# Kernel optimization log

Hardware: AMD Instinct MI355X
Metric: run time of the kernel (lower is better)

## Reference

```python
import jax, jax.numpy as jnp
import numpy as np

HEADS = 12
IDX = 0


def setup_inputs() -> dict:
    key = jax.random.key(0)
    ks = jax.random.split(key, 6)
    B, H, W, C = 16, 64, 64, 384
    x = jax.random.normal(ks[0], (B, H * W, C), dtype=jnp.float32)
    qkv_w = jax.random.normal(ks[1], (3 * C, C), dtype=jnp.float32) * 0.02
    proj_w = jax.random.normal(ks[2], (C, C), dtype=jnp.float32) * 0.02
    proj_b = jax.random.normal(ks[3], (C,), dtype=jnp.float32) * 0.02
    lepe_w = jax.random.normal(ks[4], (C, 1, 3, 3), dtype=jnp.float32) * 0.02  # depthwise, torch OIHW with I=1
    lepe_b = jax.random.normal(ks[5], (C,), dtype=jnp.float32) * 0.02
    return {"x": x, "qkv_w": qkv_w, "proj_w": proj_w, "proj_b": proj_b,
            "lepe_w": lepe_w, "lepe_b": lepe_b, "H": H, "W": W}


def _lepe_forward(x, qkv_w, proj_w, proj_b, lepe_w, lepe_b, H, W):
    B, N, C = x.shape
    hd = C // HEADS
    scale = hd ** (-0.5)
    x_img = x.reshape(B, H, W, C)

    if IDX == 0:
        # vertical strips: attend over H within each column
        x_split = jnp.transpose(x_img, (0, 2, 1, 3)).reshape(B * W, H, C)
    else:
        x_split = x_img.reshape(B * H, W, C)
    S, L, _ = x_split.shape

    qkv = (x_split @ qkv_w.T).reshape(S, L, 3, HEADS, hd)
    qkv = jnp.transpose(qkv, (2, 0, 3, 1, 4))  # (3, S, heads, L, hd)
    q, k, v = qkv[0], qkv[1], qkv[2]

    attn = jnp.einsum('shld,shmd->shlm', q, k) * scale
    attn = jax.nn.softmax(attn, axis=-1)
    out = jnp.einsum('shlm,shmd->shld', attn, v)           # (S, heads, L, hd)
    out = jnp.transpose(out, (0, 2, 1, 3)).reshape(S, L, C)
    # faithful to torch: view(B, out_H, out_W, C).view(B, H*W, C) -- no permute back for idx==0
    out_flat = out.reshape(B, H * W, C)

    # depthwise 3x3 conv LePE on the original (H, W) layout
    lepe = jax.lax.conv_general_dilated(
        jnp.transpose(x_img, (0, 3, 1, 2)), lepe_w,
        window_strides=(1, 1), padding='SAME',
        feature_group_count=C,
        dimension_numbers=('NCHW', 'OIHW', 'NCHW'))
    lepe = lepe + lepe_b[None, :, None, None]
    lepe = jnp.transpose(lepe, (0, 2, 3, 1)).reshape(B, H * W, C)

    return (out_flat + lepe) @ proj_w.T + proj_b


def reference(x, qkv_w, proj_w, proj_b, lepe_w, lepe_b, H, W):
    return _lepe_forward(x, qkv_w, proj_w, proj_b, lepe_w, lepe_b, H, W)
```

## Files before the change

### kernel.cpp

```cpp
#include <hip/hip_runtime.h>


typedef _Float16 f16;
typedef _Float16 f16x2 __attribute__((ext_vector_type(2)));
typedef _Float16 f16x8 __attribute__((ext_vector_type(8)));
typedef float    f32x4 __attribute__((ext_vector_type(4)));

__device__ __forceinline__ f32x4 mfma_16x16x32(f16x8 a, f16x8 b, f32x4 c) {
  return __builtin_amdgcn_mfma_f32_16x16x32_f16(a, b, c, 0, 0, 0);
}

__device__ __forceinline__ void gl_lds16(const f16* g, f16* l) {
  __builtin_amdgcn_global_load_lds((const __attribute__((address_space(1))) void*)g,
                                   (__attribute__((address_space(3))) void*)l, 16, 0, 0);
}

__global__ __launch_bounds__(256) void k_cvt(const float* __restrict__ src,
                                             f16* __restrict__ dst, int n8) {
  int i = blockIdx.x * 256 + threadIdx.x;
  if (i >= n8) return;
  const f32x4* s4 = (const f32x4*)src;
  f32x4 a = s4[2 * i], b = s4[2 * i + 1];
  f16x8 o;
#pragma unroll
  for (int j = 0; j < 4; ++j) { o[j] = (f16)a[j]; o[4 + j] = (f16)b[j]; }
  *(f16x8*)&dst[(long)i * 8] = o;
}

__global__ __launch_bounds__(256) void k_prep(const float* __restrict__ x,
                                              const float* __restrict__ lw,
                                              const float* __restrict__ lb,
                                              f16* __restrict__ x16,
                                              f16* __restrict__ lepe16) {
  __shared__ float ws[9 * 384];
  __shared__ float bs[384];
  for (int i = threadIdx.x; i < 3456; i += 256) {
    int c = i / 9, tap = i - c * 9;
    ws[tap * 384 + (c & 7) * 48 + (c >> 3)] = lw[i];
  }
  for (int i = threadIdx.x; i < 384; i += 256)
    bs[(i & 7) * 48 + (i >> 3)] = lb[i];
  __syncthreads();

  int chunk = blockIdx.x * 256 + threadIdx.x;
  int token = chunk / 48;
  int c0 = (chunk - token * 48) * 8;
  int cg = c0 >> 3;
  int b = token >> 12, n = token & 4095, h = n >> 6, w = n & 63;
  const float* xb = x + (long)(b << 12) * 384;

  float a8[8];
#pragma unroll
  for (int cc = 0; cc < 8; ++cc) a8[cc] = bs[cc * 48 + cg];
  f16x8 cv;
#pragma unroll
  for (int ky = 0; ky < 3; ++ky) {
    int hh = h + ky - 1;
    if (hh < 0 || hh > 63) continue;
#pragma unroll
    for (int kx = 0; kx < 3; ++kx) {
      int ww = w + kx - 1;
      if (ww < 0 || ww > 63) continue;
      const float* p = xb + (long)((hh << 6) + ww) * 384 + c0;
      float4 u = *(const float4*)p;
      float4 v = *(const float4*)(p + 4);
      float xs[8] = {u.x, u.y, u.z, u.w, v.x, v.y, v.z, v.w};
      if (ky == 1 && kx == 1) {
#pragma unroll
        for (int cc = 0; cc < 8; ++cc) cv[cc] = (f16)xs[cc];
      }
      int tap = ky * 3 + kx;
#pragma unroll
      for (int cc = 0; cc < 8; ++cc)
        a8[cc] += xs[cc] * ws[tap * 384 + cc * 48 + cg];
    }
  }
  f16x8 o;
#pragma unroll
  for (int cc = 0; cc < 8; ++cc) o[cc] = (f16)a8[cc];
  *(f16x8*)&x16[(long)token * 384 + c0] = cv;
  *(f16x8*)&lepe16[(long)token * 384 + c0] = o;
}

__global__ __launch_bounds__(512) void k_qkv(const f16* __restrict__ A,
                                             const f16* __restrict__ Bt,
                                             f16* __restrict__ C) {
  __shared__ alignas(16) f16 smem[49152];
  f16* ebuf = smem;
  const int tid = threadIdx.x;
  const int lane = tid & 63;
  const int wave = tid >> 6;
  const int wr = wave >> 1, wc = wave & 1;
  const int ln = lane & 15, quad = lane >> 4;
  const int bid = blockIdx.x;
  const int xcd = bid & 7;
  const int s = bid >> 3;
  const int mq = s / 9;
  const int mt = xcd * 32 + mq;
  const int nt = s - mq * 9;
  const long m0 = (long)mt * 256;
  const int n0 = nt * 128;

  auto stage = [&](int buf, int k0) {
    f16* Asb = smem + buf * 16384;
    f16* Bsb = smem + 32768 + buf * 8192;
#pragma unroll
    for (int r = 0; r < 4; ++r) {
      int flat = r * 512 + tid;
      int row = flat >> 3, c8 = flat & 7;
      int sc8 = (c8 ^ (row & 7)) * 8;
      gl_lds16(&A[(m0 + row) * 384 + k0 + sc8], &Asb[flat * 8]);
    }
#pragma unroll
    for (int r = 0; r < 2; ++r) {
      int flat = r * 512 + tid;
      int row = flat >> 3, c8 = flat & 7;
      int sc8 = (c8 ^ (row & 7)) * 8;
      gl_lds16(&Bt[(long)(n0 + row) * 384 + k0 + sc8], &Bsb[flat * 8]);
    }
  };

  f32x4 acc[4][4] = {};
  stage(0, 0);
  __syncthreads();
  int cur = 0;
  for (int t = 0; t < 6; ++t) {
    if (t < 5) stage(cur ^ 1, (t + 1) * 64);
    const f16* Ac = smem + cur * 16384;
    const f16* Bc = smem + 32768 + cur * 8192;
#pragma unroll
    for (int ks = 0; ks < 2; ++ks) {
      f16x8 a[4], b[4];
#pragma unroll
      for (int i = 0; i < 4; ++i)
        a[i] = *(const f16x8*)&Ac[(wr * 64 + i * 16 + ln) * 64 +
                                  ((ks * 4 + quad) ^ (ln & 7)) * 8];
#pragma unroll
      for (int j = 0; j < 4; ++j)
        b[j] = *(const f16x8*)&Bc[(wc * 64 + j * 16 + ln) * 64 +
                                  ((ks * 4 + quad) ^ (ln & 7)) * 8];
#pragma unroll
      for (int i = 0; i < 4; ++i)
#pragma unroll
        for (int j = 0; j < 4; ++j)
          acc[i][j] = mfma_16x16x32(a[i], b[j], acc[i][j]);
    }
    __syncthreads();
    cur ^= 1;
  }

  for (int p = 0; p < 2; ++p) {
    if ((wr >> 1) == p) {
      const int lr0 = (wr & 1) * 64;
#pragma unroll
      for (int i = 0; i < 4; ++i)
#pragma unroll
        for (int j = 0; j < 4; ++j)
#pragma unroll
          for (int r = 0; r < 4; ++r)
            ebuf[(lr0 + i * 16 + quad * 4 + r) * 136 + wc * 64 + j * 16 + ln] =
                (f16)acc[i][j][r];
    }
    __syncthreads();
#pragma unroll
    for (int it = 0; it < 4; ++it) {
      int flat = it * 512 + tid;
      int row = flat >> 4;
      int c8 = flat & 15;
      int t = (int)m0 + p * 128 + row;
      int nn = t & 4095;
      long prow = (long)(t & ~4095) + ((nn & 63) << 6) + (nn >> 6);
      *(f16x8*)&C[prow * 1152 + n0 + c8 * 8] =
          *(const f16x8*)&ebuf[row * 136 + c8 * 8];
    }
    __syncthreads();
  }
}

__global__ __launch_bounds__(256, 2) void k_attnproj(const f16* __restrict__ qkv,
                                                     const f16* __restrict__ lepe16,
                                                     const f16* __restrict__ pw,
                                                     const float* __restrict__ bias,
                                                     float* __restrict__ outf) {
  __shared__ alignas(16) f16 shp[4][7424];
  __shared__ alignas(16) f16 aschunk[2][64 * 40];
  const int lane = threadIdx.x & 63;
  const int wave = threadIdx.x >> 6;
  const int ln = lane & 15, quad = lane >> 4, q8 = quad * 8;
  const int b = blockIdx.x >> 6, w = blockIdx.x & 63;
  const long sbase = (long)b * 4096 + (long)w * 64;

  f16* qs = shp[wave];
  f16* ks = shp[wave] + 2560;
  f16* vt = shp[wave] + 5120;
  f16* ps = shp[wave];
  const float qscale = 0.17677669529663687f;

  f16x2 ph0[16], ph1[16], ph2[16];

  for (int hi = 0; hi < 3; ++hi) {
    const int hh = wave * 3 + hi;
#pragma unroll
    for (int r = 0; r < 4; ++r) {
      int flat = r * 64 + lane;
      int l = flat >> 2, dg = (flat & 3) * 8;
      long ta = (sbase + l) * 1152 + hh * 32 + dg;
      f16x8 qv = *(const f16x8*)&qkv[ta];
      f16x8 kv = *(const f16x8*)&qkv[ta + 384];
      f16x8 vv = *(const f16x8*)&qkv[ta + 768];
#pragma unroll
      for (int ii = 0; ii < 8; ++ii) qv[ii] = (f16)((float)qv[ii] * qscale);
      *(f16x8*)&qs[l * 40 + dg] = qv;
      *(f16x8*)&ks[l * 40 + dg] = kv;
#pragma unroll
      for (int ii = 0; ii < 8; ++ii) vt[(dg + ii) * 72 + l] = vv[ii];
    }
    f16x8 aq[4], bk[4];
#pragma unroll
    for (int i = 0; i < 4; ++i) aq[i] = *(const f16x8*)&qs[(i * 16 + ln) * 40 + q8];
#pragma unroll
    for (int j = 0; j < 4; ++j) bk[j] = *(const f16x8*)&ks[(j * 16 + ln) * 40 + q8];
    f32x4 sc[4][4] = {};
#pragma unroll
    for (int i = 0; i < 4; ++i)
#pragma unroll
      for (int j = 0; j < 4; ++j) sc[i][j] = mfma_16x16x32(aq[i], bk[j], sc[i][j]);

    float rs[4][4];
#pragma unroll
    for (int i = 0; i < 4; ++i)
#pragma unroll
      for (int r = 0; r < 4; ++r) {
        float m = -1e30f;
#pragma unroll
        for (int j = 0; j < 4; ++j) m = fmaxf(m, sc[i][j][r]);
#pragma unroll
        for (int off = 1; off < 16; off <<= 1) m = fmaxf(m, __shfl_xor(m, off, 64));
        float sum = 0.f;
#pragma unroll
        for (int j = 0; j < 4; ++j) {
          float p = __expf(sc[i][j][r] - m);
          sc[i][j][r] = p;
          sum += p;
        }
#pragma unroll
        for (int off = 1; off < 16; off <<= 1) sum += __shfl_xor(sum, off, 64);
        rs[i][r] = 1.0f / sum;
      }

#pragma unroll
    for (int i = 0; i < 4; ++i)
#pragma unroll
      for (int j = 0; j < 4; ++j)
#pragma unroll
        for (int r = 0; r < 4; ++r)
          ps[(i * 16 + quad * 4 + r) * 72 + j * 16 + ln] = (f16)sc[i][j][r];

    f32x4 oc[4][2] = {};
#pragma unroll
    for (int k2 = 0; k2 < 2; ++k2) {
      f16x8 ap[4], bv[2];
#pragma unroll
      for (int i = 0; i < 4; ++i)
        ap[i] = *(const f16x8*)&ps[(i * 16 + ln) * 72 + k2 * 32 + q8];
#pragma unroll
      for (int j = 0; j < 2; ++j)
        bv[j] = *(const f16x8*)&vt[(j * 16 + ln) * 72 + k2 * 32 + q8];
#pragma unroll
      for (int i = 0; i < 4; ++i)
#pragma unroll
        for (int j = 0; j < 2; ++j) oc[i][j] = mfma_16x16x32(ap[i], bv[j], oc[i][j]);
    }

#pragma unroll
    for (int i = 0; i < 4; ++i)
#pragma unroll
      for (int r = 0; r < 4; ++r) {
        f16x2 pk;
        pk[0] = (f16)(oc[i][0][r] * rs[i][r]);
        pk[1] = (f16)(oc[i][1][r] * rs[i][r]);
        if (hi == 0) ph0[i * 4 + r] = pk;
        else if (hi == 1) ph1[i * 4 + r] = pk;
        else ph2[i * 4 + r] = pk;
      }
  }

#define WRITECHUNK(BI, PH)                                        \
  {                                                               \
    _Pragma("unroll") for (int i = 0; i < 4; ++i)                 \
        _Pragma("unroll") for (int r = 0; r < 4; ++r) {           \
      int row = i * 16 + quad * 4 + r;                            \
      aschunk[BI][row * 40 + ln] = PH[i * 4 + r][0];              \
      aschunk[BI][row * 40 + 16 + ln] = PH[i * 4 + r][1];         \
    }                                                             \
  }

  if (wave == 0) WRITECHUNK(0, ph0);
  __syncthreads();

  f32x4 pacc[4][6] = {};
  const int ncol0 = wave * 96;
#pragma unroll
  for (int c = 0; c < 12; ++c) {
    if (c + 1 < 12 && (c + 1) / 3 == wave) {
      const int h = (c + 1) % 3;
      if (h == 0) WRITECHUNK((c + 1) & 1, ph0)
      else if (h == 1) WRITECHUNK((c + 1) & 1, ph1)
      else WRITECHUNK((c + 1) & 1, ph2)
    }
    const f16* ac = aschunk[c & 1];
    f16x8 afr[4], bfr[6];
#pragma unroll
    for (int i = 0; i < 4; ++i) {
      f16x8 av = *(const f16x8*)&ac[(i * 16 + ln) * 40 + q8];
      f16x8 lv = *(const f16x8*)&lepe16[(sbase + i * 16 + ln) * 384 + c * 32 + q8];
      afr[i] = av + lv;
    }
#pragma unroll
    for (int j = 0; j < 6; ++j)
      bfr[j] = *(const f16x8*)&pw[(long)(ncol0 + j * 16 + ln) * 384 + c * 32 + q8];
#pragma unroll
    for (int i = 0; i < 4; ++i)
#pragma unroll
      for (int j = 0; j < 6; ++j)
        pacc[i][j] = mfma_16x16x32(afr[i], bfr[j], pacc[i][j]);
    __syncthreads();
  }
#undef WRITECHUNK

  float* ebuf = (float*)&shp[0][0];
#pragma unroll
  for (int p = 0; p < 2; ++p) {
    __syncthreads();
#pragma unroll
    for (int ii = 0; ii < 2; ++ii)
#pragma unroll
      for (int j = 0; j < 6; ++j)
#pragma unroll
        for (int r = 0; r < 4; ++r)
          ebuf[(ii * 16 + quad * 4 + r) * 388 + ncol0 + j * 16 + ln] =
              pacc[p * 2 + ii][j][r];
    __syncthreads();
#pragma unroll
    for (int it = 0; it < 12; ++it) {
      int flat = it * 256 + threadIdx.x;
      int row = flat / 96;
      int c4 = flat - row * 96;
      long gr = sbase + p * 32 + row;
      int col = c4 * 4;
      float4 b4 = *(const float4*)&bias[col];
      float4 o = *(const float4*)&ebuf[row * 388 + col];
      o.x += b4.x; o.y += b4.y; o.z += b4.z; o.w += b4.w;
      *(float4*)&outf[gr * 384 + col] = o;
    }
  }
}

extern "C" void kernel_launch(void* const* d_in, const int* in_sizes, int n_in,
                              void* d_out, int out_size, void* d_ws, size_t ws_size,
                              hipStream_t stream) {
  const float* x = (const float*)d_in[0];
  const float* qkv_w = (const float*)d_in[1];
  const float* proj_w = (const float*)d_in[2];
  const float* proj_b = (const float*)d_in[3];
  const float* lepe_w = (const float*)d_in[4];
  const float* lepe_b = (const float*)d_in[5];
  float* out = (float*)d_out;

  char* ws = (char*)d_ws;
  f16* w16 = (f16*)(ws + 0);
  f16* pw16 = (f16*)(ws + 884736);
  f16* x16 = (f16*)(ws + 1179648);
  f16* lepe16 = (f16*)(ws + 51511296);
  f16* qkv16 = (f16*)(ws + 101842944);

  k_cvt<<<216, 256, 0, stream>>>(qkv_w, w16, 55296);
  k_cvt<<<72, 256, 0, stream>>>(proj_w, pw16, 18432);
  k_prep<<<12288, 256, 0, stream>>>(x, lepe_w, lepe_b, x16, lepe16);
  k_qkv<<<2304, 512, 0, stream>>>(x16, w16, qkv16);
  k_attnproj<<<1024, 256, 0, stream>>>(qkv16, lepe16, pw16, proj_b, out);
}
```

Measured before the change: 461.1 us.

## Register-prefetch qkv and projection operands, swizzle V transpose, raise MFMA priority

The per-head q/k/v global loads are now double-buffered in registers, so the next head's data is fetched while the current head computes. The projection loop does the same for its lepe and weight fragments, prefetching the next K-chunk before the current MFMAs. The transposed V store in LDS gets an XOR swizzle on the sequence index to cut bank conflicts. The MFMA blocks are wrapped in s_setprio. All of this raises register pressure, which may lower occupancy or cause spills.

```diff
diff --git a/kernel.cpp b/kernel.cpp
--- a/kernel.cpp
+++ b/kernel.cpp
@@ -196,24 +196,48 @@
   f16* ps = shp[wave];
   const float qscale = 0.17677669529663687f;
 
+  const int lrow = lane >> 2;
+  const int ldg = (lane & 3) * 8;
+  const int lswz = lane & 3;
+
   f16x2 ph0[16], ph1[16], ph2[16];
 
+  f16x8 rq[2][4], rk[2][4], rv[2][4];
+#pragma unroll
+  for (int r = 0; r < 4; ++r) {
+    int l = r * 16 + lrow;
+    long ta = (sbase + l) * 1152 + (wave * 3) * 32 + ldg;
+    rq[0][r] = *(const f16x8*)&qkv[ta];
+    rk[0][r] = *(const f16x8*)&qkv[ta + 384];
+    rv[0][r] = *(const f16x8*)&qkv[ta + 768];
+  }
+
+#pragma unroll
   for (int hi = 0; hi < 3; ++hi) {
     const int hh = wave * 3 + hi;
+    const int cb = hi & 1;
 #pragma unroll
     for (int r = 0; r < 4; ++r) {
-      int flat = r * 64 + lane;
-      int l = flat >> 2, dg = (flat & 3) * 8;
-      long ta = (sbase + l) * 1152 + hh * 32 + dg;
-      f16x8 qv = *(const f16x8*)&qkv[ta];
-      f16x8 kv = *(const f16x8*)&qkv[ta + 384];
-      f16x8 vv = *(const f16x8*)&qkv[ta + 768];
+      int l = r * 16 + lrow;
+      f16x8 qv = rq[cb][r];
 #pragma unroll
       for (int ii = 0; ii < 8; ++ii) qv[ii] = (f16)((float)qv[ii] * qscale);
-      *(f16x8*)&qs[l * 40 + dg] = qv;
-      *(f16x8*)&ks[l * 40 + dg] = kv;
-#pragma unroll
-      for (int ii = 0; ii < 8; ++ii) vt[(dg + ii) * 72 + l] = vv[ii];
+      *(f16x8*)&qs[l * 40 + ldg] = qv;
+      *(f16x8*)&ks[l * 40 + ldg] = rk[cb][r];
+      int g = l >> 3, o = l & 7;
+#pragma unroll
+      for (int ii = 0; ii < 8; ++ii)
+        vt[(ldg + ii) * 72 + (((g ^ lswz) << 3) | o)] = rv[cb][r][ii];
+    }
+    if (hi < 2) {
+#pragma unroll
+      for (int r = 0; r < 4; ++r) {
+        int l = r * 16 + lrow;
+        long ta = (sbase + l) * 1152 + (hh + 1) * 32 + ldg;
+        rq[cb ^ 1][r] = *(const f16x8*)&qkv[ta];
+        rk[cb ^ 1][r] = *(const f16x8*)&qkv[ta + 384];
+        rv[cb ^ 1][r] = *(const f16x8*)&qkv[ta + 768];
+      }
     }
     f16x8 aq[4], bk[4];
 #pragma unroll
@@ -221,10 +245,12 @@
 #pragma unroll
     for (int j = 0; j < 4; ++j) bk[j] = *(const f16x8*)&ks[(j * 16 + ln) * 40 + q8];
     f32x4 sc[4][4] = {};
+    __builtin_amdgcn_s_setprio(1);
 #pragma unroll
     for (int i = 0; i < 4; ++i)
 #pragma unroll
       for (int j = 0; j < 4; ++j) sc[i][j] = mfma_16x16x32(aq[i], bk[j], sc[i][j]);
+    __builtin_amdgcn_s_setprio(0);
 
     float rs[4][4];
 #pragma unroll
@@ -264,12 +290,17 @@
       for (int i = 0; i < 4; ++i)
         ap[i] = *(const f16x8*)&ps[(i * 16 + ln) * 72 + k2 * 32 + q8];
 #pragma unroll
-      for (int j = 0; j < 2; ++j)
-        bv[j] = *(const f16x8*)&vt[(j * 16 + ln) * 72 + k2 * 32 + q8];
+      for (int j = 0; j < 2; ++j) {
+        int dimj = j * 16 + ln;
+        bv[j] = *(const f16x8*)&vt[dimj * 72 +
+                                   (((k2 * 4 + quad) ^ ((dimj >> 3) & 7)) << 3)];
+      }
+      __builtin_amdgcn_s_setprio(1);
 #pragma unroll
       for (int i = 0; i < 4; ++i)
 #pragma unroll
         for (int j = 0; j < 2; ++j) oc[i][j] = mfma_16x16x32(ap[i], bv[j], oc[i][j]);
+      __builtin_amdgcn_s_setprio(0);
     }
 
 #pragma unroll
@@ -296,34 +327,51 @@
   }
 
   if (wave == 0) WRITECHUNK(0, ph0);
+
+  const int ncol0 = wave * 96;
+  f16x8 plv[2][4], pbf[2][6];
+#pragma unroll
+  for (int i = 0; i < 4; ++i)
+    plv[0][i] = *(const f16x8*)&lepe16[(sbase + i * 16 + ln) * 384 + q8];
+#pragma unroll
+  for (int j = 0; j < 6; ++j)
+    pbf[0][j] = *(const f16x8*)&pw[(long)(ncol0 + j * 16 + ln) * 384 + q8];
   __syncthreads();
 
   f32x4 pacc[4][6] = {};
-  const int ncol0 = wave * 96;
 #pragma unroll
   for (int c = 0; c < 12; ++c) {
+    const int cb = c & 1;
+    if (c + 1 < 12) {
+#pragma unroll
+      for (int i = 0; i < 4; ++i)
+        plv[cb ^ 1][i] =
+            *(const f16x8*)&lepe16[(sbase + i * 16 + ln) * 384 + (c + 1) * 32 + q8];
+#pragma unroll
+      for (int j = 0; j < 6; ++j)
+        pbf[cb ^ 1][j] =
+            *(const f16x8*)&pw[(long)(ncol0 + j * 16 + ln) * 384 + (c + 1) * 32 + q8];
+    }
     if (c + 1 < 12 && (c + 1) / 3 == wave) {
       const int h = (c + 1) % 3;
       if (h == 0) WRITECHUNK((c + 1) & 1, ph0)
       else if (h == 1) WRITECHUNK((c + 1) & 1, ph1)
       else WRITECHUNK((c + 1) & 1, ph2)
     }
-    const f16* ac = aschunk[c & 1];
-    f16x8 afr[4], bfr[6];
+    const f16* ac = aschunk[cb];
+    f16x8 afr[4];
 #pragma unroll
     for (int i = 0; i < 4; ++i) {
       f16x8 av = *(const f16x8*)&ac[(i * 16 + ln) * 40 + q8];
-      f16x8 lv = *(const f16x8*)&lepe16[(sbase + i * 16 + ln) * 384 + c * 32 + q8];
-      afr[i] = av + lv;
-    }
-#pragma unroll
-    for (int j = 0; j < 6; ++j)
-      bfr[j] = *(const f16x8*)&pw[(long)(ncol0 + j * 16 + ln) * 384 + c * 32 + q8];
+      afr[i] = av + plv[cb][i];
+    }
+    __builtin_amdgcn_s_setprio(1);
 #pragma unroll
     for (int i = 0; i < 4; ++i)
 #pragma unroll
       for (int j = 0; j < 6; ++j)
-        pacc[i][j] = mfma_16x16x32(afr[i], bfr[j], pacc[i][j]);
+        pacc[i][j] = mfma_16x16x32(afr[i], pbf[cb][j], pacc[i][j]);
+    __builtin_amdgcn_s_setprio(0);
     __syncthreads();
   }
 #undef WRITECHUNK
```

New measurement: 674.4 us. 1.46x slower.

## Prefetch LePE chunks into LDS asynchronously, swizzle V transpose, add MFMA priority

Applied to the files above, without the earlier changes.

In the projection loop, the per-chunk LePE tile is now loaded with async global-to-LDS transfers into a double buffer, issued one chunk ahead. This overlaps the load with the current chunk's MFMAs instead of reading global memory directly in the inner loop. The transposed V buffer in LDS gets an XOR swizzle to cut bank conflicts on the scattered writes. s_setprio is raised around the MFMA blocks. Extra LDS use could reduce occupancy, and the buffer reuse depends on the existing barrier per chunk for correctness.

```diff
diff --git a/kernel.cpp b/kernel.cpp
--- a/kernel.cpp
+++ b/kernel.cpp
@@ -184,6 +184,7 @@
                                                      float* __restrict__ outf) {
   __shared__ alignas(16) f16 shp[4][7424];
   __shared__ alignas(16) f16 aschunk[2][64 * 40];
+  __shared__ alignas(16) f16 lbuf[2][64 * 32];
   const int lane = threadIdx.x & 63;
   const int wave = threadIdx.x >> 6;
   const int ln = lane & 15, quad = lane >> 4, q8 = quad * 8;
@@ -212,8 +213,10 @@
       for (int ii = 0; ii < 8; ++ii) qv[ii] = (f16)((float)qv[ii] * qscale);
       *(f16x8*)&qs[l * 40 + dg] = qv;
       *(f16x8*)&ks[l * 40 + dg] = kv;
-#pragma unroll
-      for (int ii = 0; ii < 8; ++ii) vt[(dg + ii) * 72 + l] = vv[ii];
+      int g = l >> 3, o = l & 7, sw = dg >> 3;
+#pragma unroll
+      for (int ii = 0; ii < 8; ++ii)
+        vt[(dg + ii) * 72 + (((g ^ sw) << 3) | o)] = vv[ii];
     }
     f16x8 aq[4], bk[4];
 #pragma unroll
@@ -221,10 +224,12 @@
 #pragma unroll
     for (int j = 0; j < 4; ++j) bk[j] = *(const f16x8*)&ks[(j * 16 + ln) * 40 + q8];
     f32x4 sc[4][4] = {};
+    __builtin_amdgcn_s_setprio(1);
 #pragma unroll
     for (int i = 0; i < 4; ++i)
 #pragma unroll
       for (int j = 0; j < 4; ++j) sc[i][j] = mfma_16x16x32(aq[i], bk[j], sc[i][j]);
+    __builtin_amdgcn_s_setprio(0);
 
     float rs[4][4];
 #pragma unroll
@@ -264,12 +269,17 @@
       for (int i = 0; i < 4; ++i)
         ap[i] = *(const f16x8*)&ps[(i * 16 + ln) * 72 + k2 * 32 + q8];
 #pragma unroll
-      for (int j = 0; j < 2; ++j)
-        bv[j] = *(const f16x8*)&vt[(j * 16 + ln) * 72 + k2 * 32 + q8];
+      for (int j = 0; j < 2; ++j) {
+        int dimj = j * 16 + ln;
+        bv[j] = *(const f16x8*)&vt[dimj * 72 +
+                                   (((k2 * 4 + quad) ^ (dimj >> 3)) << 3)];
+      }
+      __builtin_amdgcn_s_setprio(1);
 #pragma unroll
       for (int i = 0; i < 4; ++i)
 #pragma unroll
         for (int j = 0; j < 2; ++j) oc[i][j] = mfma_16x16x32(ap[i], bv[j], oc[i][j]);
+      __builtin_amdgcn_s_setprio(0);
     }
 
 #pragma unroll
@@ -295,6 +305,11 @@
     }                                                             \
   }
 
+  {
+    int row = threadIdx.x >> 2, g = threadIdx.x & 3;
+    gl_lds16(&lepe16[(sbase + row) * 384 + ((g ^ (row & 3)) * 8)],
+             &lbuf[0][0] + (size_t)threadIdx.x * 8);
+  }
   if (wave == 0) WRITECHUNK(0, ph0);
   __syncthreads();
 
@@ -302,28 +317,37 @@
   const int ncol0 = wave * 96;
 #pragma unroll
   for (int c = 0; c < 12; ++c) {
-    if (c + 1 < 12 && (c + 1) / 3 == wave) {
-      const int h = (c + 1) % 3;
-      if (h == 0) WRITECHUNK((c + 1) & 1, ph0)
-      else if (h == 1) WRITECHUNK((c + 1) & 1, ph1)
-      else WRITECHUNK((c + 1) & 1, ph2)
-    }
-    const f16* ac = aschunk[c & 1];
+    const int cb = c & 1;
+    if (c + 1 < 12) {
+      int row = threadIdx.x >> 2, g = threadIdx.x & 3;
+      gl_lds16(&lepe16[(sbase + row) * 384 + (c + 1) * 32 + ((g ^ (row & 3)) * 8)],
+               &lbuf[cb ^ 1][0] + (size_t)threadIdx.x * 8);
+      if ((c + 1) / 3 == wave) {
+        const int h = (c + 1) % 3;
+        if (h == 0) WRITECHUNK(cb ^ 1, ph0)
+        else if (h == 1) WRITECHUNK(cb ^ 1, ph1)
+        else WRITECHUNK(cb ^ 1, ph2)
+      }
+    }
+    const f16* ac = aschunk[cb];
     f16x8 afr[4], bfr[6];
 #pragma unroll
     for (int i = 0; i < 4; ++i) {
-      f16x8 av = *(const f16x8*)&ac[(i * 16 + ln) * 40 + q8];
-      f16x8 lv = *(const f16x8*)&lepe16[(sbase + i * 16 + ln) * 384 + c * 32 + q8];
+      int R = i * 16 + ln;
+      f16x8 av = *(const f16x8*)&ac[R * 40 + q8];
+      f16x8 lv = *(const f16x8*)&lbuf[cb][R * 32 + ((quad ^ (R & 3)) * 8)];
       afr[i] = av + lv;
     }
 #pragma unroll
     for (int j = 0; j < 6; ++j)
       bfr[j] = *(const f16x8*)&pw[(long)(ncol0 + j * 16 + ln) * 384 + c * 32 + q8];
+    __builtin_amdgcn_s_setprio(1);
 #pragma unroll
     for (int i = 0; i < 4; ++i)
 #pragma unroll
       for (int j = 0; j < 6; ++j)
         pacc[i][j] = mfma_16x16x32(afr[i], bfr[j], pacc[i][j]);
+    __builtin_amdgcn_s_setprio(0);
     __syncthreads();
   }
 #undef WRITECHUNK
```

After: 441.9 us. 4.1% less time.
